# Performance work log

Measured on AMD Instinct MI355X. Metric: run time of the kernel, lower is better.

## Reference

```python
import jax, jax.numpy as jnp
import numpy as np

S, V, P_LEN, O_LEN = 512, 50257, 512, 128


def setup_inputs() -> dict:
    key = jax.random.key(0)
    ks = jax.random.split(key, 9)
    logits = jax.random.normal(ks[0], (S, V), jnp.float32) * 4.0
    prompt_tokens = jax.random.randint(ks[1], (S, P_LEN), 0, V, dtype=jnp.int32)
    output_tokens = jax.random.randint(ks[2], (S, O_LEN), 0, V, dtype=jnp.int32)
    presence_penalties = jax.random.uniform(ks[3], (S,), jnp.float32) * 2.0
    frequency_penalties = jax.random.uniform(ks[4], (S,), jnp.float32) * 2.0
    repetition_penalties = 1.0 + jax.random.uniform(ks[5], (S,), jnp.float32) * 0.3
    top_ps = 0.5 + jax.random.uniform(ks[6], (S,), jnp.float32) * 0.5
    top_ks = jax.random.randint(ks[7], (S,), 1, 1025, dtype=jnp.int32)
    min_ps = jax.random.uniform(ks[8], (S,), jnp.float32) * 0.05
    return {
        'logits': logits,
        'prompt_tokens': prompt_tokens,
        'output_tokens': output_tokens,
        'presence_penalties': presence_penalties,
        'frequency_penalties': frequency_penalties,
        'repetition_penalties': repetition_penalties,
        'top_ps': top_ps,
        'top_ks': top_ks,
        'min_ps': min_ps,
    }


def _bin_counts_and_mask(tokens, vocab_size):
    # scatter-add bincount per row, same math as torch scatter_add_ version
    n = tokens.shape[0]
    counts = jnp.zeros((n, vocab_size), jnp.int32)
    counts = counts.at[jnp.arange(n)[:, None], tokens].add(1)
    return counts, counts > 0


def _sampler_forward(logits, prompt_tokens, output_tokens,
                     presence_penalties, frequency_penalties, repetition_penalties,
                     top_ps, top_ks, min_ps):
    vocab_size = logits.shape[-1]
    neg_inf = jnp.float32(-jnp.inf)

    # ---- _apply_penalties ----
    _, prompt_mask = _bin_counts_and_mask(prompt_tokens, vocab_size)
    output_bin_counts, output_mask = _bin_counts_and_mask(output_tokens, vocab_size)
    seen = prompt_mask | output_mask
    rep = jnp.where(seen, repetition_penalties[:, None], 1.0)
    logits = jnp.where(logits > 0, logits / rep, logits * rep)
    logits = logits - frequency_penalties[:, None] * output_bin_counts.astype(logits.dtype)
    logits = logits - presence_penalties[:, None] * output_mask.astype(logits.dtype)

    # ---- _apply_top_p_top_k ---- (descending sort + cumsum + unsort gather)
    order = jnp.argsort(-logits, axis=-1)                       # [S, V] descending
    logits_sort = jnp.take_along_axis(logits, order, axis=-1)
    probs_sort = jax.nn.softmax(logits_sort, axis=-1)
    probs_sum = jnp.cumsum(probs_sort, axis=-1)
    top_p_mask = (probs_sum - probs_sort) > top_ps[:, None]
    top_k_mask = jnp.arange(vocab_size)[None, :] >= top_ks[:, None]
    logits_sort = jnp.where(top_p_mask | top_k_mask, neg_inf, logits_sort)
    inv = jnp.argsort(order, axis=-1)                           # inverse permutation
    logits = jnp.take_along_axis(logits_sort, inv, axis=-1)

    # ---- _apply_min_p ----
    probs = jax.nn.softmax(logits, axis=-1)
    top_probs = jnp.max(probs, axis=-1, keepdims=True)
    scaled_min_p = min_ps[:, None] * top_probs
    logits = jnp.where(probs < scaled_min_p, neg_inf, logits)
    return logits


def reference(logits, prompt_tokens, output_tokens, presence_penalties,
              frequency_penalties, repetition_penalties, top_ps, top_ks, min_ps):
    return _sampler_forward(logits, prompt_tokens, output_tokens,
                            presence_penalties, frequency_penalties,
                            repetition_penalties, top_ps, top_ks, min_ps)
```

## Files before the change

### kernel.cpp

```cpp
#include <hip/hip_runtime.h>
#include <hip/hip_fp16.h>
#include <math.h>

#define S_ROWS 512
#define VOCAB 50257
#define P_LEN 512
#define O_LEN 128
#define NBW 1571
#define NH 256
#define NHIST 2048
#define CAP 4096
#define SCAP 1536
#define NT 1024
#define L2E 1.4426950408889634f
#define CUTF 6.0f
typedef unsigned long long ull;

#define MASK_VAL (-3.3895313892515355e38f)
#define EXP2(x) __builtin_amdgcn_exp2f(x)

__device__ __forceinline__ float fin(float v) {
  return (v == v && v >= -3.0e38f && v <= 3.0e38f) ? v : MASK_VAL;
}
__device__ __forceinline__ unsigned fkey(float x) {
  unsigned b = __float_as_uint(x);
  return (b & 0x80000000u) ? ~b : (b | 0x80000000u);
}
__device__ __forceinline__ float unfkey(unsigned u) {
  unsigned b = (u & 0x80000000u) ? (u & 0x7fffffffu) : ~u;
  return __uint_as_float(b);
}
__device__ __forceinline__ unsigned key16(float x) {
  unsigned short b = __half_as_ushort(__float2half(x));
  return (b & 0x8000) ? (unsigned)(unsigned short)(~b) : (unsigned)(b | 0x8000u);
}
__device__ __forceinline__ unsigned hashcnt(int v, const unsigned* hkey, const unsigned* hcnt) {
  unsigned h = ((unsigned)v * 2654435761u) >> 24;
  for (;;) {
    unsigned k = hkey[h];
    if (k == (unsigned)v) return hcnt[h];
    if (k == 0xffffffffu) return 0u;
    h = (h + 1) & (NH - 1);
  }
}
__device__ __forceinline__ float penS(float l, int v, const unsigned* bm,
                                      float rp, float rinv, float fp, float pp,
                                      const unsigned* hkey, const unsigned* hcnt) {
  unsigned sw = bm[2 * (v >> 5)], ow = bm[2 * (v >> 5) + 1];
  bool seen = (sw >> (v & 31)) & 1u;
  float x = seen ? ((l > 0.0f) ? l * rinv : l * rp) : l;
  if ((ow >> (v & 31)) & 1u)
    x = (x - fp * (float)hashcnt(v, hkey, hcnt)) - pp;
  return x;
}

#define SUFFIX_SELECT(tgt, out_bin_slot, out_cntgt_slot)                     \
  if (wid == 0) {                                                            \
    int base = lane * 32;                                                    \
    unsigned S = 0;                                                          \
    for (int b = 0; b < 32; ++b) S += hist[base + b];                        \
    unsigned T = S;                                                          \
    for (int off = 1; off < 64; off <<= 1) {                                 \
      unsigned t = __shfl_down(T, off);                                      \
      if (lane + off < 64) T += t;                                           \
    }                                                                        \
    unsigned Tnext = T - S;                                                  \
    if (T >= (tgt) && Tnext < (tgt)) {                                       \
      unsigned acc = Tnext;                                                  \
      for (int b = 31; b >= 0; --b) {                                        \
        unsigned h = hist[base + b];                                         \
        acc += h;                                                            \
        if (acc >= (tgt)) {                                                  \
          scal_i[out_bin_slot] = base + b;                                   \
          scal_i[out_cntgt_slot] = (int)(acc - h);                           \
          break;                                                             \
        }                                                                    \
      }                                                                      \
    }                                                                        \
  }

__global__ __launch_bounds__(NT, 8) void sampler_kernel_r11(
    const float* __restrict__ logits,
    const int* __restrict__ prompt_toks,
    const int* __restrict__ output_toks,
    const float* __restrict__ presence,
    const float* __restrict__ frequency,
    const float* __restrict__ repetition,
    const float* __restrict__ top_ps,
    const int* __restrict__ top_ks,
    const float* __restrict__ min_ps,
    float* __restrict__ out)
{
  __shared__ unsigned bm[2 * NBW];
  __shared__ unsigned hkey[NH];
  __shared__ unsigned hcnt[NH];
  __shared__ unsigned hist[NHIST];
  __shared__ __align__(16) ull cand[CAP];
  __shared__ __align__(16) ull skey[SCAP + 2];
  __shared__ float reds[16];
  __shared__ unsigned wscan[16];
  __shared__ unsigned sub[32];
  __shared__ int scal_i[8];
  __shared__ float scal_f[4];

  unsigned* offs = (unsigned*)cand;
  ull* srt = (ull*)((char*)cand + 8192);
  unsigned short* sbin2 = (unsigned short*)((char*)cand + 20480);
  float* se = (float*)((char*)cand + 23552);

  const int row = blockIdx.x;
  const int tid = threadIdx.x;
  const int lane = tid & 63, wid = tid >> 6;

  for (int i = tid; i < 2 * NBW; i += NT) bm[i] = 0u;
  for (int i = tid; i < NH; i += NT) { hkey[i] = 0xffffffffu; hcnt[i] = 0u; }
  for (int i = tid; i < NHIST; i += NT) hist[i] = 0u;
  if (tid < 8) scal_i[tid] = 0;
  if (tid < 32) sub[tid] = 0u;
  __syncthreads();

  if (tid < P_LEN) {
    int t = prompt_toks[row * P_LEN + tid];
    if (t >= 0 && t < VOCAB) atomicOr(&bm[2 * (t >> 5)], 1u << (t & 31));
  }
  if (tid < O_LEN) {
    int t = output_toks[row * O_LEN + tid];
    if (t >= 0 && t < VOCAB) {
      atomicOr(&bm[2 * (t >> 5)], 1u << (t & 31));
      atomicOr(&bm[2 * (t >> 5) + 1], 1u << (t & 31));
      unsigned h = ((unsigned)t * 2654435761u) >> 24;
      for (;;) {
        unsigned prev = atomicCAS(&hkey[h], 0xffffffffu, (unsigned)t);
        if (prev == 0xffffffffu || prev == (unsigned)t) { atomicAdd(&hcnt[h], 1u); break; }
        h = (h + 1) & (NH - 1);
      }
    }
  }
  __syncthreads();

  const float rp = repetition[row];
  const float rinv = __frcp_rn(rp);
  const float fp = frequency[row];
  const float pp = presence[row];
  const float tp = top_ps[row];
  const float mp = min_ps[row];
  int K = top_ks[row];
  if (K < 1) K = 1;
  if (K > 1024) K = 1024;
  const unsigned Ku = (unsigned)K;

  const float* lrow = logits + (size_t)row * VOCAB;
  float* orow = out + (size_t)row * VOCAB;

  const int head = (4 - (row & 3)) & 3;
  const int nq = (VOCAB - head) >> 2;
  const int tail_start = head + (nq << 2);

  const float4* lq4 = (const float4*)(lrow + head);
  float4* oq = (float4*)(orow + head);
  const float4 mq = make_float4(MASK_VAL, MASK_VAL, MASK_VAL, MASK_VAL);

  float z0 = 0.0f, z1 = 0.0f;
  for (int i = tid; i < nq; i += NT) {
    float4 q = lq4[i];
    int v0 = head + (i << 2);
    int wA = v0 >> 5, wB = (v0 + 3) >> 5;
    unsigned sh = (unsigned)(v0 & 31);
    uint2 pA = *(const uint2*)&bm[2 * wA];
    uint2 pB = *(const uint2*)&bm[2 * wB];
    unsigned swin = (unsigned)(((((ull)pB.x) << 32) | pA.x) >> sh);
    unsigned owin = (unsigned)(((((ull)pB.y) << 32) | pA.y) >> sh);
    float f0 = ((swin >> 0) & 1) ? ((q.x > 0.0f) ? rinv : rp) : 1.0f;
    float f1 = ((swin >> 1) & 1) ? ((q.y > 0.0f) ? rinv : rp) : 1.0f;
    float f2 = ((swin >> 2) & 1) ? ((q.z > 0.0f) ? rinv : rp) : 1.0f;
    float f3 = ((swin >> 3) & 1) ? ((q.w > 0.0f) ? rinv : rp) : 1.0f;
    float x0 = q.x * f0, x1 = q.y * f1, x2 = q.z * f2, x3 = q.w * f3;
    if (owin & 15u) {
      if ((owin >> 0) & 1) x0 = (x0 - fp * (float)hashcnt(v0 + 0, hkey, hcnt)) - pp;
      if ((owin >> 1) & 1) x1 = (x1 - fp * (float)hashcnt(v0 + 1, hkey, hcnt)) - pp;
      if ((owin >> 2) & 1) x2 = (x2 - fp * (float)hashcnt(v0 + 2, hkey, hcnt)) - pp;
      if ((owin >> 3) & 1) x3 = (x3 - fp * (float)hashcnt(v0 + 3, hkey, hcnt)) - pp;
    }
    if (x0 >= CUTF) { int p = atomicAdd(&scal_i[3], 1); if (p < CAP) cand[p] = (((ull)(~fkey(x0))) << 32) | (unsigned)(v0 + 0); }
    if (x1 >= CUTF) { int p = atomicAdd(&scal_i[3], 1); if (p < CAP) cand[p] = (((ull)(~fkey(x1))) << 32) | (unsigned)(v0 + 1); }
    if (x2 >= CUTF) { int p = atomicAdd(&scal_i[3], 1); if (p < CAP) cand[p] = (((ull)(~fkey(x2))) << 32) | (unsigned)(v0 + 2); }
    if (x3 >= CUTF) { int p = atomicAdd(&scal_i[3], 1); if (p < CAP) cand[p] = (((ull)(~fkey(x3))) << 32) | (unsigned)(v0 + 3); }
    z0 += EXP2(x0 * L2E) + EXP2(x2 * L2E);
    z1 += EXP2(x1 * L2E) + EXP2(x3 * L2E);
    oq[i] = mq;
  }
  for (int v = tid; v < head; v += NT) {
    float x = penS(lrow[v], v, bm, rp, rinv, fp, pp, hkey, hcnt);
    if (x >= CUTF) { int p = atomicAdd(&scal_i[3], 1); if (p < CAP) cand[p] = (((ull)(~fkey(x))) << 32) | (unsigned)v; }
    z0 += EXP2(x * L2E);
    orow[v] = MASK_VAL;
  }
  for (int v = tail_start + tid; v < VOCAB; v += NT) {
    float x = penS(lrow[v], v, bm, rp, rinv, fp, pp, hkey, hcnt);
    if (x >= CUTF) { int p = atomicAdd(&scal_i[3], 1); if (p < CAP) cand[p] = (((ull)(~fkey(x))) << 32) | (unsigned)v; }
    z1 += EXP2(x * L2E);
    orow[v] = MASK_VAL;
  }
  float zl = z0 + z1;
  for (int off = 32; off > 0; off >>= 1) zl += __shfl_down(zl, off);
  if (lane == 0) reds[wid] = zl;
  __syncthreads();
  if (tid == 0) {
    float z = 0.0f;
    for (int w2 = 0; w2 < 16; ++w2) z += reds[w2];
    scal_f[1] = z;
  }
  __syncthreads();
  const float Z = scal_f[1];
  int M1 = scal_i[3];

  if (M1 < (int)Ku || M1 > CAP) {
    for (int v = tid; v < VOCAB; v += NT) {
      float x = penS(lrow[v], v, bm, rp, rinv, fp, pp, hkey, hcnt);
      atomicAdd(&hist[key16(x) >> 5], 1u);
    }
    __syncthreads();
    SUFFIX_SELECT(Ku, 5, 6)
    __syncthreads();
    const unsigned thrF = ((unsigned)scal_i[5]) << 5;
    if (tid == 0) scal_i[3] = 0;
    for (int i = tid; i < NHIST; i += NT) hist[i] = 0u;
    __syncthreads();
    for (int v = tid; v < VOCAB; v += NT) {
      float x = penS(lrow[v], v, bm, rp, rinv, fp, pp, hkey, hcnt);
      if (key16(x) >= thrF) {
        int p = atomicAdd(&scal_i[3], 1);
        if (p < CAP) cand[p] = (((ull)(~fkey(x))) << 32) | (unsigned)v;
      }
    }
    __syncthreads();
    M1 = scal_i[3];
  }
  if (M1 > CAP) M1 = CAP;

  for (int c = tid; c < M1; c += NT) {
    float x = unfkey(~((unsigned)(cand[c] >> 32)));
    atomicAdd(&hist[key16(x) >> 5], 1u);
  }
  __syncthreads();
  SUFFIX_SELECT(Ku, 0, 2)
  __syncthreads();
  const unsigned bA = (unsigned)scal_i[0];

  for (int c = tid; c < M1; c += NT) {
    float x = unfkey(~((unsigned)(cand[c] >> 32)));
    unsigned k = key16(x);
    if ((k >> 5) == bA) atomicAdd(&sub[k & 31u], 1u);
  }
  __syncthreads();
  if (tid == 0) {
    unsigned acc = 0, Cgt = (unsigned)scal_i[2];
    int chosen = 0;
    for (int b = 31; b >= 0; --b) {
      acc += sub[b];
      if (Cgt + acc >= Ku) { chosen = b; break; }
    }
    scal_i[4] = (int)((bA << 5) | (unsigned)chosen);
    scal_i[7] = 0;
  }
  __syncthreads();
  const unsigned thr16 = (unsigned)scal_i[4];

  for (int c = tid; c < M1; c += NT) {
    ull e = cand[c];
    float x = unfkey(~((unsigned)(e >> 32)));
    if (key16(x) >= thr16) {
      int p = atomicAdd(&scal_i[7], 1);
      if (p < SCAP) skey[p] = e;
    }
  }
  __syncthreads();
  int M2 = scal_i[7]; if (M2 > SCAP) M2 = SCAP;

  for (int i = tid; i < NHIST; i += NT) hist[i] = 0u;
  if (tid < 1024) se[tid] = 0.0f;
  __syncthreads();
  for (int c = tid; c < M2; c += NT) {
    float x = unfkey(~((unsigned)(skey[c] >> 32)));
    unsigned d = key16(x) - thr16; if (d > 2047u) d = 2047u;
    atomicAdd(&hist[d], 1u);
  }
  __syncthreads();
  {
    int j0 = 2 * tid, j1 = 2 * tid + 1;
    unsigned a0 = hist[2047 - j0], a1 = hist[2047 - j1];
    unsigned sc = a0 + a1;
    unsigned inc = sc;
    for (int off = 1; off < 64; off <<= 1) {
      unsigned t = __shfl_up(inc, off);
      if (lane >= off) inc += t;
    }
    if (lane == 63) wscan[wid] = inc;
    __syncthreads();
    if (tid == 0) {
      unsigned run = 0;
      for (int w2 = 0; w2 < 16; ++w2) { unsigned t = wscan[w2]; wscan[w2] = run; run += t; }
    }
    __syncthreads();
    unsigned excl = wscan[wid] + (inc - sc);
    offs[2047 - j0] = excl;
    offs[2047 - j1] = excl + a0;
  }
  __syncthreads();
  for (int i = tid; i < NHIST; i += NT) hist[i] = 0u;
  __syncthreads();
  for (int c = tid; c < M2; c += NT) {
    ull k = skey[c];
    float x = unfkey(~((unsigned)(k >> 32)));
    unsigned d = key16(x) - thr16; if (d > 2047u) d = 2047u;
    unsigned slot = offs[d] + atomicAdd(&hist[d], 1u);
    srt[slot] = k;
    sbin2[slot] = (unsigned short)d;
  }
  __syncthreads();
  {
    int s0 = tid, s1 = tid + NT;
    ull k0 = 0, k1 = 0; int t0 = -1, t1 = -1;
    if (s0 < M2) {
      k0 = srt[s0];
      unsigned d = sbin2[s0];
      unsigned lo = offs[d], n = hist[d];
      int r = 0;
      if (n > 1u) for (unsigned u = 0; u < n; ++u) r += (srt[lo + u] < k0) ? 1 : 0;
      t0 = (int)lo + r;
    }
    if (s1 < M2) {
      k1 = srt[s1];
      unsigned d = sbin2[s1];
      unsigned lo = offs[d], n = hist[d];
      int r = 0;
      if (n > 1u) for (unsigned u = 0; u < n; ++u) r += (srt[lo + u] < k1) ? 1 : 0;
      t1 = (int)lo + r;
    }
    __syncthreads();
    if (t0 >= 0) {
      srt[t0] = k0;
      if (t0 < 1024) se[t0] = EXP2(unfkey(~((unsigned)(k0 >> 32))) * L2E);
    }
    if (t1 >= 0) {
      srt[t1] = k1;
      if (t1 < 1024) se[t1] = EXP2(unfkey(~((unsigned)(k1 >> 32))) * L2E);
    }
  }
  __syncthreads();

  float e_t = (tid < K) ? se[tid] : 0.0f;
  float csum = e_t;
  for (int off = 1; off < 64; off <<= 1) {
    float t = __shfl_up(csum, off);
    if (lane >= off) csum += t;
  }
  if (lane == 63) reds[wid] = csum;
  __syncthreads();
  if (tid == 0) {
    float a = 0.0f;
    for (int w2 = 0; w2 < 16; ++w2) { float t = reds[w2]; reds[w2] = a; a += t; }
  }
  __syncthreads();
  const float cum = csum + reds[wid];
  const float cb = cum - e_t;
  const float tpZ = tp * Z;
  const bool kp = (tid < K) && !(cb > tpZ);
  if (kp) {
    float e = se[tid];
    if (!(e < mp * se[0])) {
      ull key = srt[tid];
      unsigned v = (unsigned)(key & 0xffffffffu);
      if (v < (unsigned)VOCAB) orow[v] = fin(unfkey(~((unsigned)(key >> 32))));
    }
  }
}

extern "C" void kernel_launch(void* const* d_in, const int* in_sizes, int n_in,
                              void* d_out, int out_size, void* d_ws, size_t ws_size,
                              hipStream_t stream) {
  const float* logits = (const float*)d_in[0];
  const int* pt  = (const int*)d_in[1];
  const int* ot  = (const int*)d_in[2];
  const float* pres = (const float*)d_in[3];
  const float* freq = (const float*)d_in[4];
  const float* rep  = (const float*)d_in[5];
  const float* tps  = (const float*)d_in[6];
  const int* tks    = (const int*)d_in[7];
  const float* mps  = (const float*)d_in[8];
  float* out = (float*)d_out;

  hipLaunchKernelGGL(sampler_kernel_r11, dim3(S_ROWS), dim3(NT), 0, stream,
                     logits, pt, ot, pres, freq, rep, tps, tks, mps, out);
}
```

Before: 50.15 us.

## Replace two-level top-k radix select with a single offset histogram over packed candidates

Candidates are now stored as 32-bit records, a 16-bit value key plus a 16-bit vocab index, instead of 64-bit full-key entries. The coarse histogram, sub-bin refinement and compaction passes are replaced by one 2048-bin histogram anchored at the cutoff key. Its suffix scan directly yields the threshold bin and the scatter offsets. Survivors have their exact penalized value recomputed from global logits before the in-bin rank sort. The main streaming loop also handles two float4 chunks per iteration for more memory-level parallelism. The aim is fewer LDS passes and barriers, at the cost of extra global re-reads, more shared memory (buffers no longer aliased), and clamping of very large keys into the top bin.

```diff
diff --git a/kernel.cpp b/kernel.cpp
--- a/kernel.cpp
+++ b/kernel.cpp
@@ -79,7 +79,34 @@
     }                                                                        \
   }
 
-__global__ __launch_bounds__(NT, 8) void sampler_kernel_r11(
+#define PROC4(qv, v0g, STORE_OK)                                             \
+  {                                                                          \
+    int wA = (v0g) >> 5, wB = ((v0g) + 3) >> 5;                              \
+    unsigned sh = (unsigned)((v0g) & 31);                                    \
+    uint2 pA = *(const uint2*)&bm[2 * wA];                                   \
+    uint2 pB = *(const uint2*)&bm[2 * wB];                                   \
+    unsigned swin = (unsigned)(((((ull)pB.x) << 32) | pA.x) >> sh);          \
+    unsigned owin = (unsigned)(((((ull)pB.y) << 32) | pA.y) >> sh);          \
+    float f0 = ((swin >> 0) & 1) ? ((qv.x > 0.0f) ? rinv : rp) : 1.0f;       \
+    float f1 = ((swin >> 1) & 1) ? ((qv.y > 0.0f) ? rinv : rp) : 1.0f;       \
+    float f2 = ((swin >> 2) & 1) ? ((qv.z > 0.0f) ? rinv : rp) : 1.0f;       \
+    float f3 = ((swin >> 3) & 1) ? ((qv.w > 0.0f) ? rinv : rp) : 1.0f;       \
+    float x0 = qv.x * f0, x1 = qv.y * f1, x2 = qv.z * f2, x3 = qv.w * f3;    \
+    if (owin & 15u) {                                                        \
+      if ((owin >> 0) & 1) x0 = (x0 - fp * (float)hashcnt((v0g) + 0, hkey, hcnt)) - pp; \
+      if ((owin >> 1) & 1) x1 = (x1 - fp * (float)hashcnt((v0g) + 1, hkey, hcnt)) - pp; \
+      if ((owin >> 2) & 1) x2 = (x2 - fp * (float)hashcnt((v0g) + 2, hkey, hcnt)) - pp; \
+      if ((owin >> 3) & 1) x3 = (x3 - fp * (float)hashcnt((v0g) + 3, hkey, hcnt)) - pp; \
+    }                                                                        \
+    if (x0 >= CUTF) { int p = atomicAdd(&scal_i[3], 1); if (p < CAP) cand[p] = (key16(x0) << 16) | (unsigned)((v0g) + 0); } \
+    if (x1 >= CUTF) { int p = atomicAdd(&scal_i[3], 1); if (p < CAP) cand[p] = (key16(x1) << 16) | (unsigned)((v0g) + 1); } \
+    if (x2 >= CUTF) { int p = atomicAdd(&scal_i[3], 1); if (p < CAP) cand[p] = (key16(x2) << 16) | (unsigned)((v0g) + 2); } \
+    if (x3 >= CUTF) { int p = atomicAdd(&scal_i[3], 1); if (p < CAP) cand[p] = (key16(x3) << 16) | (unsigned)((v0g) + 3); } \
+    z0 += EXP2(x0 * L2E) + EXP2(x2 * L2E);                                   \
+    z1 += EXP2(x1 * L2E) + EXP2(x3 * L2E);                                   \
+  }
+
+__global__ __launch_bounds__(NT, 8) void sampler_kernel_r12(
     const float* __restrict__ logits,
     const int* __restrict__ prompt_toks,
     const int* __restrict__ output_toks,
@@ -95,18 +122,15 @@
   __shared__ unsigned hkey[NH];
   __shared__ unsigned hcnt[NH];
   __shared__ unsigned hist[NHIST];
-  __shared__ __align__(16) ull cand[CAP];
-  __shared__ __align__(16) ull skey[SCAP + 2];
+  __shared__ unsigned offs[NHIST];
+  __shared__ unsigned cand[CAP];
+  __shared__ __align__(16) ull srt[SCAP];
+  __shared__ unsigned short sbin[SCAP];
+  __shared__ float se[1024];
   __shared__ float reds[16];
   __shared__ unsigned wscan[16];
-  __shared__ unsigned sub[32];
   __shared__ int scal_i[8];
   __shared__ float scal_f[4];
-
-  unsigned* offs = (unsigned*)cand;
-  ull* srt = (ull*)((char*)cand + 8192);
-  unsigned short* sbin2 = (unsigned short*)((char*)cand + 20480);
-  float* se = (float*)((char*)cand + 23552);
 
   const int row = blockIdx.x;
   const int tid = threadIdx.x;
@@ -116,7 +140,6 @@
   for (int i = tid; i < NH; i += NT) { hkey[i] = 0xffffffffu; hcnt[i] = 0u; }
   for (int i = tid; i < NHIST; i += NT) hist[i] = 0u;
   if (tid < 8) scal_i[tid] = 0;
-  if (tid < 32) sub[tid] = 0u;
   __syncthreads();
 
   if (tid < P_LEN) {
@@ -148,6 +171,7 @@
   if (K < 1) K = 1;
   if (K > 1024) K = 1024;
   const unsigned Ku = (unsigned)K;
+  const unsigned base16 = key16(CUTF);
 
   const float* lrow = logits + (size_t)row * VOCAB;
   float* orow = out + (size_t)row * VOCAB;
@@ -161,43 +185,28 @@
   const float4 mq = make_float4(MASK_VAL, MASK_VAL, MASK_VAL, MASK_VAL);
 
   float z0 = 0.0f, z1 = 0.0f;
-  for (int i = tid; i < nq; i += NT) {
-    float4 q = lq4[i];
-    int v0 = head + (i << 2);
-    int wA = v0 >> 5, wB = (v0 + 3) >> 5;
-    unsigned sh = (unsigned)(v0 & 31);
-    uint2 pA = *(const uint2*)&bm[2 * wA];
-    uint2 pB = *(const uint2*)&bm[2 * wB];
-    unsigned swin = (unsigned)(((((ull)pB.x) << 32) | pA.x) >> sh);
-    unsigned owin = (unsigned)(((((ull)pB.y) << 32) | pA.y) >> sh);
-    float f0 = ((swin >> 0) & 1) ? ((q.x > 0.0f) ? rinv : rp) : 1.0f;
-    float f1 = ((swin >> 1) & 1) ? ((q.y > 0.0f) ? rinv : rp) : 1.0f;
-    float f2 = ((swin >> 2) & 1) ? ((q.z > 0.0f) ? rinv : rp) : 1.0f;
-    float f3 = ((swin >> 3) & 1) ? ((q.w > 0.0f) ? rinv : rp) : 1.0f;
-    float x0 = q.x * f0, x1 = q.y * f1, x2 = q.z * f2, x3 = q.w * f3;
-    if (owin & 15u) {
-      if ((owin >> 0) & 1) x0 = (x0 - fp * (float)hashcnt(v0 + 0, hkey, hcnt)) - pp;
-      if ((owin >> 1) & 1) x1 = (x1 - fp * (float)hashcnt(v0 + 1, hkey, hcnt)) - pp;
-      if ((owin >> 2) & 1) x2 = (x2 - fp * (float)hashcnt(v0 + 2, hkey, hcnt)) - pp;
-      if ((owin >> 3) & 1) x3 = (x3 - fp * (float)hashcnt(v0 + 3, hkey, hcnt)) - pp;
-    }
-    if (x0 >= CUTF) { int p = atomicAdd(&scal_i[3], 1); if (p < CAP) cand[p] = (((ull)(~fkey(x0))) << 32) | (unsigned)(v0 + 0); }
-    if (x1 >= CUTF) { int p = atomicAdd(&scal_i[3], 1); if (p < CAP) cand[p] = (((ull)(~fkey(x1))) << 32) | (unsigned)(v0 + 1); }
-    if (x2 >= CUTF) { int p = atomicAdd(&scal_i[3], 1); if (p < CAP) cand[p] = (((ull)(~fkey(x2))) << 32) | (unsigned)(v0 + 2); }
-    if (x3 >= CUTF) { int p = atomicAdd(&scal_i[3], 1); if (p < CAP) cand[p] = (((ull)(~fkey(x3))) << 32) | (unsigned)(v0 + 3); }
-    z0 += EXP2(x0 * L2E) + EXP2(x2 * L2E);
-    z1 += EXP2(x1 * L2E) + EXP2(x3 * L2E);
+  const int half = (nq + 1) >> 1;
+  for (int i = tid; i < half; i += NT) {
+    const int ib = i + half;
+    const bool hb = (ib < nq);
+    float4 qa = lq4[i];
+    float4 qb = hb ? lq4[ib] : make_float4(-1e30f, -1e30f, -1e30f, -1e30f);
+    const int v0a = head + (i << 2);
+    const int v0b = hb ? (head + (ib << 2)) : 0;
+    PROC4(qa, v0a, 1)
+    PROC4(qb, v0b, hb)
     oq[i] = mq;
+    if (hb) oq[ib] = mq;
   }
   for (int v = tid; v < head; v += NT) {
     float x = penS(lrow[v], v, bm, rp, rinv, fp, pp, hkey, hcnt);
-    if (x >= CUTF) { int p = atomicAdd(&scal_i[3], 1); if (p < CAP) cand[p] = (((ull)(~fkey(x))) << 32) | (unsigned)v; }
+    if (x >= CUTF) { int p = atomicAdd(&scal_i[3], 1); if (p < CAP) cand[p] = (key16(x) << 16) | (unsigned)v; }
     z0 += EXP2(x * L2E);
     orow[v] = MASK_VAL;
   }
   for (int v = tail_start + tid; v < VOCAB; v += NT) {
     float x = penS(lrow[v], v, bm, rp, rinv, fp, pp, hkey, hcnt);
-    if (x >= CUTF) { int p = atomicAdd(&scal_i[3], 1); if (p < CAP) cand[p] = (((ull)(~fkey(x))) << 32) | (unsigned)v; }
+    if (x >= CUTF) { int p = atomicAdd(&scal_i[3], 1); if (p < CAP) cand[p] = (key16(x) << 16) | (unsigned)v; }
     z1 += EXP2(x * L2E);
     orow[v] = MASK_VAL;
   }
@@ -228,9 +237,10 @@
     __syncthreads();
     for (int v = tid; v < VOCAB; v += NT) {
       float x = penS(lrow[v], v, bm, rp, rinv, fp, pp, hkey, hcnt);
-      if (key16(x) >= thrF) {
+      unsigned k = key16(x);
+      if (k >= thrF) {
         int p = atomicAdd(&scal_i[3], 1);
-        if (p < CAP) cand[p] = (((ull)(~fkey(x))) << 32) | (unsigned)v;
+        if (p < CAP) cand[p] = (k << 16) | (unsigned)v;
       }
     }
     __syncthreads();
@@ -239,53 +249,12 @@
   if (M1 > CAP) M1 = CAP;
 
   for (int c = tid; c < M1; c += NT) {
-    float x = unfkey(~((unsigned)(cand[c] >> 32)));
-    atomicAdd(&hist[key16(x) >> 5], 1u);
-  }
-  __syncthreads();
-  SUFFIX_SELECT(Ku, 0, 2)
-  __syncthreads();
-  const unsigned bA = (unsigned)scal_i[0];
-
-  for (int c = tid; c < M1; c += NT) {
-    float x = unfkey(~((unsigned)(cand[c] >> 32)));
-    unsigned k = key16(x);
-    if ((k >> 5) == bA) atomicAdd(&sub[k & 31u], 1u);
-  }
-  __syncthreads();
-  if (tid == 0) {
-    unsigned acc = 0, Cgt = (unsigned)scal_i[2];
-    int chosen = 0;
-    for (int b = 31; b >= 0; --b) {
-      acc += sub[b];
-      if (Cgt + acc >= Ku) { chosen = b; break; }
-    }
-    scal_i[4] = (int)((bA << 5) | (unsigned)chosen);
-    scal_i[7] = 0;
-  }
-  __syncthreads();
-  const unsigned thr16 = (unsigned)scal_i[4];
-
-  for (int c = tid; c < M1; c += NT) {
-    ull e = cand[c];
-    float x = unfkey(~((unsigned)(e >> 32)));
-    if (key16(x) >= thr16) {
-      int p = atomicAdd(&scal_i[7], 1);
-      if (p < SCAP) skey[p] = e;
-    }
-  }
-  __syncthreads();
-  int M2 = scal_i[7]; if (M2 > SCAP) M2 = SCAP;
-
-  for (int i = tid; i < NHIST; i += NT) hist[i] = 0u;
-  if (tid < 1024) se[tid] = 0.0f;
-  __syncthreads();
-  for (int c = tid; c < M2; c += NT) {
-    float x = unfkey(~((unsigned)(skey[c] >> 32)));
-    unsigned d = key16(x) - thr16; if (d > 2047u) d = 2047u;
+    int d = (int)(cand[c] >> 16) - (int)base16;
+    d = (d < 0) ? 0 : ((d > 2047) ? 2047 : d);
     atomicAdd(&hist[d], 1u);
   }
   __syncthreads();
+
   {
     int j0 = 2 * tid, j1 = 2 * tid + 1;
     unsigned a0 = hist[2047 - j0], a1 = hist[2047 - j1];
@@ -302,28 +271,43 @@
       for (int w2 = 0; w2 < 16; ++w2) { unsigned t = wscan[w2]; wscan[w2] = run; run += t; }
     }
     __syncthreads();
-    unsigned excl = wscan[wid] + (inc - sc);
-    offs[2047 - j0] = excl;
-    offs[2047 - j1] = excl + a0;
-  }
-  __syncthreads();
+    unsigned excl0 = wscan[wid] + (inc - sc);
+    unsigned excl1 = excl0 + a0;
+    offs[2047 - j0] = excl0;
+    offs[2047 - j1] = excl1;
+    if (excl0 + a0 >= Ku && excl0 < Ku) scal_i[0] = 2047 - j0;
+    if (excl1 + a1 >= Ku && excl1 < Ku) scal_i[0] = 2047 - j1;
+  }
+  __syncthreads();
+  const int thrbin = scal_i[0];
+  int M2 = (int)(offs[thrbin] + hist[thrbin]);
+  if (M2 > SCAP) M2 = SCAP;
+
   for (int i = tid; i < NHIST; i += NT) hist[i] = 0u;
   __syncthreads();
-  for (int c = tid; c < M2; c += NT) {
-    ull k = skey[c];
-    float x = unfkey(~((unsigned)(k >> 32)));
-    unsigned d = key16(x) - thr16; if (d > 2047u) d = 2047u;
-    unsigned slot = offs[d] + atomicAdd(&hist[d], 1u);
-    srt[slot] = k;
-    sbin2[slot] = (unsigned short)d;
-  }
-  __syncthreads();
+
+  for (int c = tid; c < M1; c += NT) {
+    unsigned rec = cand[c];
+    int d = (int)(rec >> 16) - (int)base16;
+    d = (d < 0) ? 0 : ((d > 2047) ? 2047 : d);
+    if (d >= thrbin) {
+      int v = (int)(rec & 0xffffu);
+      float x = penS(lrow[v], v, bm, rp, rinv, fp, pp, hkey, hcnt);
+      unsigned slot = offs[d] + atomicAdd(&hist[d], 1u);
+      if (slot < (unsigned)SCAP) {
+        srt[slot] = (((ull)(~fkey(x))) << 32) | (unsigned)v;
+        sbin[slot] = (unsigned short)d;
+      }
+    }
+  }
+  __syncthreads();
+
   {
     int s0 = tid, s1 = tid + NT;
     ull k0 = 0, k1 = 0; int t0 = -1, t1 = -1;
     if (s0 < M2) {
       k0 = srt[s0];
-      unsigned d = sbin2[s0];
+      unsigned d = sbin[s0];
       unsigned lo = offs[d], n = hist[d];
       int r = 0;
       if (n > 1u) for (unsigned u = 0; u < n; ++u) r += (srt[lo + u] < k0) ? 1 : 0;
@@ -331,18 +315,19 @@
     }
     if (s1 < M2) {
       k1 = srt[s1];
-      unsigned d = sbin2[s1];
+      unsigned d = sbin[s1];
       unsigned lo = offs[d], n = hist[d];
       int r = 0;
       if (n > 1u) for (unsigned u = 0; u < n; ++u) r += (srt[lo + u] < k1) ? 1 : 0;
       t1 = (int)lo + r;
     }
-    __syncthreads();
-    if (t0 >= 0) {
+    if (tid < 1024) se[tid] = 0.0f;
+    __syncthreads();
+    if (t0 >= 0 && t0 < SCAP) {
       srt[t0] = k0;
       if (t0 < 1024) se[t0] = EXP2(unfkey(~((unsigned)(k0 >> 32))) * L2E);
     }
-    if (t1 >= 0) {
+    if (t1 >= 0 && t1 < SCAP) {
       srt[t1] = k1;
       if (t1 < 1024) se[t1] = EXP2(unfkey(~((unsigned)(k1 >> 32))) * L2E);
     }
@@ -390,6 +375,6 @@
   const float* mps  = (const float*)d_in[8];
   float* out = (float*)d_out;
 
-  hipLaunchKernelGGL(sampler_kernel_r11, dim3(S_ROWS), dim3(NT), 0, stream,
+  hipLaunchKernelGGL(sampler_kernel_r12, dim3(S_ROWS), dim3(NT), 0, stream,
                      logits, pt, ot, pres, freq, rep, tps, tks, mps, out);
 }
```

Result: no change. 50.29 us (+0.3%).
